# Performance work log

Hardware: AMD Instinct MI355X
Metric: run time of the kernel (lower is better)

The kernel has to match this reference:

```python
import jax, jax.numpy as jnp
import numpy as np

HIDDEN = 1024
Q_OUT = 2048
KV_OUT = 1024
HEAD_DIM = 128
N_Q = Q_OUT // HEAD_DIM      # 16
N_KV = KV_OUT // HEAD_DIM    # 8
EPS = 1e-6
ROPE_BASE = 10000.0


def _rms_norm(x, w, eps=EPS):
    # normalize over last dim (head_dim)
    ms = jnp.mean(x * x, axis=-1, keepdims=True)
    return x * jax.lax.rsqrt(ms + eps) * w


def _rope_cos_sin(t, dim=HEAD_DIM, base=ROPE_BASE):
    inv_freq = 1.0 / (base ** (jnp.arange(0, dim, 2, dtype=jnp.float32) / dim))
    pos = jnp.arange(t, dtype=jnp.float32)
    freqs = pos[:, None] * inv_freq[None, :]          # (T, D/2)
    emb = jnp.concatenate([freqs, freqs], axis=-1)    # (T, D)
    return jnp.cos(emb), jnp.sin(emb)


def _rotate_half(x):
    d = x.shape[-1] // 2
    return jnp.concatenate([-x[..., d:], x[..., :d]], axis=-1)


def setup_inputs() -> dict:
    key = jax.random.key(0)
    ks = jax.random.split(key, 7)
    def lin(k, fan_in, fan_out):
        # nn.Linear default init: U(-1/sqrt(fan_in), 1/sqrt(fan_in)); stored as (in, out) for x @ W
        bound = 1.0 / np.sqrt(fan_in)
        return jax.random.uniform(k, (fan_in, fan_out), jnp.float32, -bound, bound)
    return {
        "x": jax.random.normal(ks[0], (2, 2048, HIDDEN), jnp.float32),
        "Wq": lin(ks[1], HIDDEN, Q_OUT),
        "Wk": lin(ks[2], HIDDEN, KV_OUT),
        "Wv": lin(ks[3], HIDDEN, KV_OUT),
        "Wo": lin(ks[4], Q_OUT, HIDDEN),
        "q_norm_w": jnp.ones((HEAD_DIM,), jnp.float32),
        "k_norm_w": jnp.ones((HEAD_DIM,), jnp.float32),
    }


def reference(x, Wq, Wk, Wv, Wo, q_norm_w, k_norm_w):
    b, t, _ = x.shape
    # QKV projections, shaped to (B, H, T, D)
    q = (x @ Wq).reshape(b, t, N_Q, HEAD_DIM).transpose(0, 2, 1, 3)
    k = (x @ Wk).reshape(b, t, N_KV, HEAD_DIM).transpose(0, 2, 1, 3)
    v = (x @ Wv).reshape(b, t, N_KV, HEAD_DIM).transpose(0, 2, 1, 3)
    # per-head RMSNorm on q/k
    q = _rms_norm(q, q_norm_w)
    k = _rms_norm(k, k_norm_w)
    # RoPE (positions 0..T-1)
    cos, sin = _rope_cos_sin(t)                        # (T, D)
    cos = cos[None, None]; sin = sin[None, None]       # (1,1,T,D)
    q = q * cos + _rotate_half(q) * sin
    k = k * cos + _rotate_half(k) * sin
    # GQA: repeat_interleave kv heads to match q heads
    rep = N_Q // N_KV
    k_r = jnp.repeat(k, rep, axis=1)                   # (B, Hq, T, D)
    v_r = jnp.repeat(v, rep, axis=1)
    # causal attention
    scores = jnp.einsum('bhqd,bhkd->bhqk', q, k_r) / jnp.sqrt(jnp.asarray(HEAD_DIM, x.dtype))
    causal = jnp.triu(jnp.full((t, t), -jnp.inf, dtype=scores.dtype), k=1)[None, None]
    attn = jax.nn.softmax(scores + causal, axis=-1)
    out = jnp.einsum('bhqk,bhkd->bhqd', attn, v_r)     # (B, Hq, T, D)
    out = out.transpose(0, 2, 1, 3).reshape(b, t, Q_OUT)
    return out @ Wo
```

## Files before the change

kernel.cpp:

```cpp
#include <hip/hip_runtime.h>
#include <math.h>

typedef __attribute__((ext_vector_type(8))) short short8;
typedef __attribute__((ext_vector_type(4))) float f32x4;
typedef __attribute__((ext_vector_type(4))) unsigned int uint4v;

#define HIDDEN 1024
#define QOUT 2048
#define KVOUT 1024
#define HD 128
#define TSEQ 2048

__device__ __forceinline__ float bf2f(unsigned short h) {
    union { unsigned int u; float f; } x; x.u = ((unsigned int)h) << 16; return x.f;
}
__device__ __forceinline__ unsigned short f2bf(float f) {
    union { float f; unsigned int u; } x; x.f = f;
    unsigned int r = (x.u + 0x7fffu + ((x.u >> 16) & 1u)) >> 16;
    return (unsigned short)r;
}
__device__ __forceinline__ unsigned int pk2bf(float lo, float hi) {
    return (unsigned int)f2bf(lo) | ((unsigned int)f2bf(hi) << 16);
}

__device__ __forceinline__ void glds16(const unsigned short* g, unsigned short* l) {
    __builtin_amdgcn_global_load_lds(
        (const __attribute__((address_space(1))) unsigned int*)g,
        (__attribute__((address_space(3))) unsigned int*)l, 16, 0, 0);
}

__global__ __launch_bounds__(256) void cast_f32_bf16(const float* __restrict__ in,
                                                     unsigned short* __restrict__ out, int n4) {
    int i = blockIdx.x * 256 + threadIdx.x;
    if (i >= n4) return;
    float4 v = *(const float4*)(in + (size_t)i * 4);
    unsigned short o[4] = {f2bf(v.x), f2bf(v.y), f2bf(v.z), f2bf(v.w)};
    *(unsigned long long*)(out + (size_t)i * 4) = *(unsigned long long*)o;
}

__global__ __launch_bounds__(256) void transpose_f32_bf16(const float* __restrict__ W,
                                                          unsigned short* __restrict__ Wt,
                                                          int K, int N) {
    __shared__ __attribute__((aligned(16))) unsigned short Ls[64 * 72];
    int ntiles = N >> 6;
    int kt = blockIdx.x / ntiles, nt = blockIdx.x - kt * ntiles;
    int k0 = kt * 64, n0 = nt * 64;
    int tid = threadIdx.x;
    for (int t = 0; t < 4; t++) {
        int idx = tid + t * 256;
        int r = idx >> 4, seg = idx & 15;
        float4 v = *(const float4*)(W + (size_t)(k0 + r) * N + n0 + seg * 4);
        int c = seg * 4;
        Ls[(c + 0) * 72 + r] = f2bf(v.x);
        Ls[(c + 1) * 72 + r] = f2bf(v.y);
        Ls[(c + 2) * 72 + r] = f2bf(v.z);
        Ls[(c + 3) * 72 + r] = f2bf(v.w);
    }
    __syncthreads();
    for (int t = 0; t < 2; t++) {
        int idx = tid + t * 256;
        int rr = idx >> 3, seg = idx & 7;
        uint4v v = *(const uint4v*)(Ls + rr * 72 + seg * 8);
        *(uint4v*)(Wt + (size_t)(n0 + rr) * K + k0 + seg * 8) = v;
    }
}

template <int OUT_BF16, int BN>
__global__ __launch_bounds__(256) void gemm_bt(const unsigned short* __restrict__ A,
                                               const unsigned short* __restrict__ Bt,
                                               void* __restrict__ Cout,
                                               int M, int N, int K) {
    constexpr int MT = (BN == 128) ? 4 : 2;
    __shared__ __attribute__((aligned(16))) unsigned short As[128 * 32];
    __shared__ __attribute__((aligned(16))) unsigned short Bs[BN * 32];
    const int tid = threadIdx.x;
    const int lane = tid & 63;
    const int warp = tid >> 6;
    const int ln = lane & 15;
    const int quad = lane >> 4;
    const int wm = (BN == 128) ? (warp >> 1) : warp;
    const int wn = (BN == 128) ? (warp & 1) : 0;
    const int m0 = blockIdx.y * 128;
    const int n0 = blockIdx.x * BN;

    const int srow = lane >> 2;
    const int schunk = (lane & 3) ^ (srow & 3);
    const unsigned short* Ag = A + (size_t)(m0 + warp * 16 + srow) * K + schunk * 8;
    const unsigned short* Bg = Bt + (size_t)(n0 + warp * 16 + srow) * K + schunk * 8;
    unsigned short* AsW = As + warp * 16 * 32;
    unsigned short* BsW = Bs + warp * 16 * 32;

    f32x4 acc[MT][4];
    for (int i = 0; i < MT; i++)
        for (int j = 0; j < 4; j++) acc[i][j] = (f32x4){0.f, 0.f, 0.f, 0.f};

    const int rq = quad ^ (ln & 3);
    for (int k0 = 0; k0 < K; k0 += 32) {
        __syncthreads();
        glds16(Ag + k0, AsW);
        glds16(Ag + (size_t)64 * K + k0, AsW + 64 * 32);
        glds16(Bg + k0, BsW);
        if (BN == 128) glds16(Bg + (size_t)64 * K + k0, BsW + 64 * 32);
        __syncthreads();
        short8 af[MT], bf[4];
        for (int mt = 0; mt < MT; mt++)
            af[mt] = *(const short8*)(As + (wm * (MT * 16) + mt * 16 + ln) * 32 + rq * 8);
        for (int nt = 0; nt < 4; nt++)
            bf[nt] = *(const short8*)(Bs + (wn * 64 + nt * 16 + ln) * 32 + rq * 8);
        for (int mt = 0; mt < MT; mt++)
            for (int nt = 0; nt < 4; nt++)
                acc[mt][nt] = __builtin_amdgcn_mfma_f32_16x16x32_bf16(bf[nt], af[mt], acc[mt][nt], 0, 0, 0);
    }
    for (int mt = 0; mt < MT; mt++) {
        int row = m0 + wm * (MT * 16) + mt * 16 + ln;
        for (int nt = 0; nt < 4; nt++) {
            int colb = n0 + wn * 64 + nt * 16 + quad * 4;
            if (OUT_BF16) {
                unsigned long long pk =
                    (unsigned long long)pk2bf(acc[mt][nt][0], acc[mt][nt][1]) |
                    ((unsigned long long)pk2bf(acc[mt][nt][2], acc[mt][nt][3]) << 32);
                *(unsigned long long*)((unsigned short*)Cout + (size_t)row * N + colb) = pk;
            } else {
                *(f32x4*)((float*)Cout + (size_t)row * N + colb) = acc[mt][nt];
            }
        }
    }
}

__global__ __launch_bounds__(256) void norm_rope(const unsigned short* __restrict__ QKV,
                                                 const float* __restrict__ qw,
                                                 const float* __restrict__ kw,
                                                 unsigned short* __restrict__ Q,
                                                 unsigned short* __restrict__ Kb) {
    int warp = threadIdx.x >> 6;
    int lane = threadIdx.x & 63;
    int gid = blockIdx.x * 4 + warp;
    int tok = gid / 24;
    int slot = gid - tok * 24;
    int b = tok >> 11, t = tok & 2047;
    const float* w;
    unsigned short* dst;
    int col0;
    if (slot < 16) {
        col0 = slot * HD;
        dst = Q + ((size_t)(b * 16 + slot) * TSEQ + t) * HD;
        w = qw;
    } else {
        int hk = slot - 16;
        col0 = QOUT + hk * HD;
        dst = Kb + ((size_t)(b * 8 + hk) * TSEQ + t) * HD;
        w = kw;
    }
    const unsigned short* row = QKV + (size_t)tok * 4096 + col0;
    float e0 = bf2f(row[lane]), e1 = bf2f(row[lane + 64]);
    float ss = e0 * e0 + e1 * e1;
    for (int off = 1; off < 64; off <<= 1) ss += __shfl_xor(ss, off);
    float rr = rsqrtf(ss * (1.0f / 128.0f) + 1e-6f);
    float n0 = e0 * rr * w[lane];
    float n1 = e1 * rr * w[lane + 64];
    float invf = __builtin_exp2f(-(float)lane * 0.20762050593045951f);
    float ang = (float)t * invf;
    float sf, cf;
    __sincosf(ang, &sf, &cf);
    float o0 = n0 * cf - n1 * sf;
    float o1 = n1 * cf + n0 * sf;
    dst[lane] = f2bf(o0);
    dst[lane + 64] = f2bf(o1);
}

__global__ __launch_bounds__(256) void v_transpose(const unsigned short* __restrict__ QKV,
                                                   unsigned short* __restrict__ Vt) {
    __shared__ __attribute__((aligned(16))) unsigned short Ls[128 * 72];
    int bid = blockIdx.x;
    int tt = bid & 31, hk = (bid >> 5) & 7, b = bid >> 8;
    int t0 = tt * 64;
    int tid = threadIdx.x;
    const unsigned short* base = QKV + (size_t)(b * 2048 + t0) * 4096 + 3072 + hk * 128;
    for (int i = 0; i < 4; i++) {
        int idx = tid + i * 256;
        int r = idx >> 4, seg = idx & 15;
        uint4v v = *(const uint4v*)(base + (size_t)r * 4096 + seg * 8);
        unsigned short* pv = (unsigned short*)&v;
        int d = seg * 8;
        for (int jj = 0; jj < 8; jj++) Ls[(d + jj) * 72 + r] = pv[jj];
    }
    __syncthreads();
    unsigned short* out = Vt + (size_t)(b * 8 + hk) * 128 * 2048;
    for (int i = 0; i < 4; i++) {
        int idx = tid + i * 256;
        int d = idx >> 3, seg = idx & 7;
        uint4v v = *(const uint4v*)(Ls + d * 72 + seg * 8);
        *(uint4v*)(out + (size_t)d * 2048 + t0 + seg * 8) = v;
    }
}

__global__ __launch_bounds__(256, 2) void attn(const unsigned short* __restrict__ Q,
                                               const unsigned short* __restrict__ Kg,
                                               const unsigned short* __restrict__ Vt,
                                               unsigned short* __restrict__ Og) {
    __shared__ __attribute__((aligned(16))) unsigned short Ks[64 * 128];
    __shared__ __attribute__((aligned(16))) unsigned short Vs[128 * 64];
    __shared__ __attribute__((aligned(16))) unsigned short Ps[4][16 * 72];
    const int p = blockIdx.x;
    const int bh = blockIdx.y;
    const int b = bh >> 4, h = bh & 15, hk = h >> 1;
    const int tid = threadIdx.x;
    const int warp = tid >> 6, lane = tid & 63, ln = lane & 15, quad = lane >> 4;
    const int strip[2] = { p * 64 + warp * 16, (31 - p) * 64 + warp * 16 };
    const int jdiag[2] = { p, 31 - p };

    const unsigned short* Kbase = Kg + (size_t)(b * 8 + hk) * TSEQ * HD;
    const unsigned short* Vbase = Vt + (size_t)(b * 8 + hk) * HD * TSEQ;
    const unsigned short* Qh = Q + (size_t)(b * 16 + h) * TSEQ * HD;

    short8 qf[2][4];
#pragma unroll
    for (int st = 0; st < 2; st++)
#pragma unroll
        for (int kt = 0; kt < 4; kt++)
            qf[st][kt] = *(const short8*)(Qh + (size_t)(strip[st] + ln) * HD + kt * 32 + quad * 8);

    f32x4 o[2][8];
#pragma unroll
    for (int st = 0; st < 2; st++)
#pragma unroll
        for (int ot = 0; ot < 8; ot++) o[st][ot] = (f32x4){0.f, 0.f, 0.f, 0.f};
    float m_[2] = {-1e30f, -1e30f}, l_[2] = {0.f, 0.f};

    const int kr = lane >> 4;
    const int kc = lane & 15;
    const int vr = lane >> 3;
    const int vc = lane & 7;

    const float kscale = 0.12750580997495268f;
    const int nT = 32 - p;
    for (int j = 0; j < nT; j++) {
        const int j0 = j * 64;
        __syncthreads();
#pragma unroll
        for (int c = 0; c < 4; c++) {
            int row = warp * 16 + c * 4 + kr;
            glds16(Kbase + (size_t)(j0 + row) * HD + ((kc ^ (row & 15)) * 8),
                   Ks + (warp * 16 + c * 4) * 128);
        }
#pragma unroll
        for (int c = 0; c < 4; c++) {
            int d = warp * 32 + c * 8 + vr;
            glds16(Vbase + (size_t)d * TSEQ + j0 + ((vc ^ (d & 7)) * 8),
                   Vs + (warp * 32 + c * 8) * 64);
        }
        __syncthreads();
        const bool act0 = (j <= jdiag[0]);
        f32x4 s[2][4];
#pragma unroll
        for (int kb = 0; kb < 4; kb++) {
            s[0][kb] = (f32x4){0.f, 0.f, 0.f, 0.f};
            s[1][kb] = (f32x4){0.f, 0.f, 0.f, 0.f};
        }
#pragma unroll
        for (int kt = 0; kt < 4; kt++) {
            short8 kf[4];
#pragma unroll
            for (int kb = 0; kb < 4; kb++)
                kf[kb] = *(const short8*)(Ks + (kb * 16 + ln) * 128 + (((kt * 4 + quad) ^ ln) * 8));
#pragma unroll
            for (int kb = 0; kb < 4; kb++)
                s[1][kb] = __builtin_amdgcn_mfma_f32_16x16x32_bf16(kf[kb], qf[1][kt], s[1][kb], 0, 0, 0);
            if (act0)
#pragma unroll
                for (int kb = 0; kb < 4; kb++)
                    s[0][kb] = __builtin_amdgcn_mfma_f32_16x16x32_bf16(kf[kb], qf[0][kt], s[0][kb], 0, 0, 0);
        }
        short8 pf[2][2];
        float al[2] = {1.f, 1.f};
#pragma unroll
        for (int st = 0; st < 2; st++) {
            if (st == 0 && !act0) continue;
            float mx = -1e30f;
            if (j == jdiag[st]) {
                const int qloc = warp * 16 + ln;
#pragma unroll
                for (int kb = 0; kb < 4; kb++)
#pragma unroll
                    for (int r = 0; r < 4; r++) {
                        int kvloc = kb * 16 + quad * 4 + r;
                        float v = s[st][kb][r] * kscale;
                        v = (kvloc > qloc) ? -1e30f : v;
                        s[st][kb][r] = v;
                        mx = fmaxf(mx, v);
                    }
            } else {
#pragma unroll
                for (int kb = 0; kb < 4; kb++)
#pragma unroll
                    for (int r = 0; r < 4; r++) {
                        float v = s[st][kb][r] * kscale;
                        s[st][kb][r] = v;
                        mx = fmaxf(mx, v);
                    }
            }
            mx = fmaxf(mx, __shfl_xor(mx, 16));
            mx = fmaxf(mx, __shfl_xor(mx, 32));
            float mn = fmaxf(m_[st], mx);
            al[st] = __builtin_exp2f(m_[st] - mn);
            float sum = 0.f;
#pragma unroll
            for (int kb = 0; kb < 4; kb++)
#pragma unroll
                for (int r = 0; r < 4; r++) {
                    float pv = __builtin_exp2f(s[st][kb][r] - mn);
                    s[st][kb][r] = pv;
                    sum += pv;
                }
            sum += __shfl_xor(sum, 16);
            sum += __shfl_xor(sum, 32);
            m_[st] = mn;
            l_[st] = l_[st] * al[st] + sum;
#pragma unroll
            for (int kb = 0; kb < 4; kb++) {
                unsigned long long pk =
                    (unsigned long long)pk2bf(s[st][kb][0], s[st][kb][1]) |
                    ((unsigned long long)pk2bf(s[st][kb][2], s[st][kb][3]) << 32);
                *(unsigned long long*)(&Ps[warp][ln * 72 + kb * 16 + quad * 4]) = pk;
            }
            pf[st][0] = *(const short8*)(&Ps[warp][ln * 72 + quad * 8]);
            pf[st][1] = *(const short8*)(&Ps[warp][ln * 72 + 32 + quad * 8]);
        }
        if (act0 && __any(al[0] != 1.0f))
#pragma unroll
            for (int ot = 0; ot < 8; ot++)
#pragma unroll
                for (int r = 0; r < 4; r++) o[0][ot][r] *= al[0];
        if (__any(al[1] != 1.0f))
#pragma unroll
            for (int ot = 0; ot < 8; ot++)
#pragma unroll
                for (int r = 0; r < 4; r++) o[1][ot][r] *= al[1];
#pragma unroll
        for (int ot = 0; ot < 8; ot++) {
            short8 vf0 = *(const short8*)(Vs + (ot * 16 + ln) * 64 + ((quad ^ (ln & 7)) * 8));
            short8 vf1 = *(const short8*)(Vs + (ot * 16 + ln) * 64 + (((4 + quad) ^ (ln & 7)) * 8));
            o[1][ot] = __builtin_amdgcn_mfma_f32_16x16x32_bf16(vf0, pf[1][0], o[1][ot], 0, 0, 0);
            o[1][ot] = __builtin_amdgcn_mfma_f32_16x16x32_bf16(vf1, pf[1][1], o[1][ot], 0, 0, 0);
            if (act0) {
                o[0][ot] = __builtin_amdgcn_mfma_f32_16x16x32_bf16(vf0, pf[0][0], o[0][ot], 0, 0, 0);
                o[0][ot] = __builtin_amdgcn_mfma_f32_16x16x32_bf16(vf1, pf[0][1], o[0][ot], 0, 0, 0);
            }
        }
    }
#pragma unroll
    for (int st = 0; st < 2; st++) {
        float inv = 1.0f / l_[st];
        size_t rowoff = ((size_t)(b * TSEQ + strip[st] + ln)) * QOUT + h * 128 + quad * 4;
#pragma unroll
        for (int ot = 0; ot < 8; ot++) {
            unsigned long long pk =
                (unsigned long long)pk2bf(o[st][ot][0] * inv, o[st][ot][1] * inv) |
                ((unsigned long long)pk2bf(o[st][ot][2] * inv, o[st][ot][3] * inv) << 32);
            *(unsigned long long*)(Og + rowoff + ot * 16) = pk;
        }
    }
}

extern "C" void kernel_launch(void* const* d_in, const int* in_sizes, int n_in,
                              void* d_out, int out_size, void* d_ws, size_t ws_size,
                              hipStream_t stream) {
    (void)in_sizes; (void)n_in; (void)out_size;
    const float* x  = (const float*)d_in[0];
    const float* Wq = (const float*)d_in[1];
    const float* Wk = (const float*)d_in[2];
    const float* Wv = (const float*)d_in[3];
    const float* Wo = (const float*)d_in[4];
    const float* qw = (const float*)d_in[5];
    const float* kw = (const float*)d_in[6];

    char* ws = (char*)d_ws;
    const size_t MB = 1024 * 1024;
    unsigned short* Wt   = (unsigned short*)(ws);
    unsigned short* Wot  = (unsigned short*)(ws + 8 * MB);
    unsigned short* QKVb = (unsigned short*)(ws + 12 * MB);
    unsigned short* xb   = (unsigned short*)(ws + 44 * MB);
    unsigned short* Qb   = (unsigned short*)(ws + 52 * MB);
    unsigned short* Kb   = (unsigned short*)(ws + 68 * MB);
    unsigned short* Vtb  = (unsigned short*)(ws + 76 * MB);
    unsigned short* Ob   = (unsigned short*)(ws + 84 * MB);
    if (ws_size < 100 * MB) return;

    cast_f32_bf16<<<dim3(4096), 256, 0, stream>>>(x, xb, 1048576);
    transpose_f32_bf16<<<dim3(512), 256, 0, stream>>>(Wq, Wt, 1024, 2048);
    transpose_f32_bf16<<<dim3(256), 256, 0, stream>>>(Wk, Wt + (size_t)2048 * 1024, 1024, 1024);
    transpose_f32_bf16<<<dim3(256), 256, 0, stream>>>(Wv, Wt + (size_t)3072 * 1024, 1024, 1024);
    transpose_f32_bf16<<<dim3(512), 256, 0, stream>>>(Wo, Wot, 2048, 1024);
    gemm_bt<1, 128><<<dim3(32, 32), 256, 0, stream>>>(xb, Wt, QKVb, 4096, 4096, 1024);
    norm_rope<<<dim3(24576), 256, 0, stream>>>(QKVb, qw, kw, Qb, Kb);
    v_transpose<<<dim3(512), 256, 0, stream>>>(QKVb, Vtb);
    attn<<<dim3(16, 32), 256, 0, stream>>>(Qb, Kb, Vtb, Ob);
    gemm_bt<0, 64><<<dim3(16, 32), 256, 0, stream>>>(Ob, Wot, (float*)d_out, 4096, 1024, 2048);
}
```

Measured before the change: 300.9 us.

## Double-buffer LDS in GEMM and attention and merge small prep kernels

```diff
diff --git a/kernel.cpp b/kernel.cpp
--- a/kernel.cpp
+++ b/kernel.cpp
@@ -29,23 +29,33 @@
         (__attribute__((address_space(3))) unsigned int*)l, 16, 0, 0);
 }
 
-__global__ __launch_bounds__(256) void cast_f32_bf16(const float* __restrict__ in,
-                                                     unsigned short* __restrict__ out, int n4) {
-    int i = blockIdx.x * 256 + threadIdx.x;
-    if (i >= n4) return;
-    float4 v = *(const float4*)(in + (size_t)i * 4);
-    unsigned short o[4] = {f2bf(v.x), f2bf(v.y), f2bf(v.z), f2bf(v.w)};
-    *(unsigned long long*)(out + (size_t)i * 4) = *(unsigned long long*)o;
-}
-
-__global__ __launch_bounds__(256) void transpose_f32_bf16(const float* __restrict__ W,
-                                                          unsigned short* __restrict__ Wt,
-                                                          int K, int N) {
+__global__ __launch_bounds__(256) void prep(const float* __restrict__ x,
+                                            const float* __restrict__ Wq,
+                                            const float* __restrict__ Wk,
+                                            const float* __restrict__ Wv,
+                                            const float* __restrict__ Wo,
+                                            unsigned short* __restrict__ xb,
+                                            unsigned short* __restrict__ Wt,
+                                            unsigned short* __restrict__ Wot) {
+    int bid = blockIdx.x;
+    int tid = threadIdx.x;
+    if (bid < 4096) {
+        int i = bid * 256 + tid;
+        float4 v = *(const float4*)(x + (size_t)i * 4);
+        unsigned short o[4] = {f2bf(v.x), f2bf(v.y), f2bf(v.z), f2bf(v.w)};
+        *(unsigned long long*)(xb + (size_t)i * 4) = *(unsigned long long*)o;
+        return;
+    }
+    bid -= 4096;
+    const float* W; unsigned short* D; int K, N;
+    if (bid < 512)       { W = Wq; D = Wt;                          K = 1024; N = 2048; }
+    else if (bid < 768)  { bid -= 512;  W = Wk; D = Wt + (size_t)2048 * 1024; K = 1024; N = 1024; }
+    else if (bid < 1024) { bid -= 768;  W = Wv; D = Wt + (size_t)3072 * 1024; K = 1024; N = 1024; }
+    else                 { bid -= 1024; W = Wo; D = Wot;                      K = 2048; N = 1024; }
     __shared__ __attribute__((aligned(16))) unsigned short Ls[64 * 72];
     int ntiles = N >> 6;
-    int kt = blockIdx.x / ntiles, nt = blockIdx.x - kt * ntiles;
+    int kt = bid / ntiles, nt = bid - kt * ntiles;
     int k0 = kt * 64, n0 = nt * 64;
-    int tid = threadIdx.x;
     for (int t = 0; t < 4; t++) {
         int idx = tid + t * 256;
         int r = idx >> 4, seg = idx & 15;
@@ -61,7 +71,7 @@
         int idx = tid + t * 256;
         int rr = idx >> 3, seg = idx & 7;
         uint4v v = *(const uint4v*)(Ls + rr * 72 + seg * 8);
-        *(uint4v*)(Wt + (size_t)(n0 + rr) * K + k0 + seg * 8) = v;
+        *(uint4v*)(D + (size_t)(n0 + rr) * K + k0 + seg * 8) = v;
     }
 }
 
@@ -71,8 +81,8 @@
                                                void* __restrict__ Cout,
                                                int M, int N, int K) {
     constexpr int MT = (BN == 128) ? 4 : 2;
-    __shared__ __attribute__((aligned(16))) unsigned short As[128 * 32];
-    __shared__ __attribute__((aligned(16))) unsigned short Bs[BN * 32];
+    __shared__ __attribute__((aligned(16))) unsigned short As[2][128 * 32];
+    __shared__ __attribute__((aligned(16))) unsigned short Bs[2][BN * 32];
     const int tid = threadIdx.x;
     const int lane = tid & 63;
     const int warp = tid >> 6;
@@ -87,32 +97,45 @@
     const int schunk = (lane & 3) ^ (srow & 3);
     const unsigned short* Ag = A + (size_t)(m0 + warp * 16 + srow) * K + schunk * 8;
     const unsigned short* Bg = Bt + (size_t)(n0 + warp * 16 + srow) * K + schunk * 8;
-    unsigned short* AsW = As + warp * 16 * 32;
-    unsigned short* BsW = Bs + warp * 16 * 32;
 
     f32x4 acc[MT][4];
+#pragma unroll
     for (int i = 0; i < MT; i++)
+#pragma unroll
         for (int j = 0; j < 4; j++) acc[i][j] = (f32x4){0.f, 0.f, 0.f, 0.f};
 
+    auto stage = [&](int k0, int bi) {
+        glds16(Ag + k0, As[bi] + warp * 16 * 32);
+        glds16(Ag + (size_t)64 * K + k0, As[bi] + warp * 16 * 32 + 64 * 32);
+        glds16(Bg + k0, Bs[bi] + warp * 16 * 32);
+        if (BN == 128) glds16(Bg + (size_t)64 * K + k0, Bs[bi] + warp * 16 * 32 + 64 * 32);
+    };
+
     const int rq = quad ^ (ln & 3);
-    for (int k0 = 0; k0 < K; k0 += 32) {
+    const int KI = K >> 5;
+    stage(0, 0);
+    for (int it = 0; it < KI; it++) {
         __syncthreads();
-        glds16(Ag + k0, AsW);
-        glds16(Ag + (size_t)64 * K + k0, AsW + 64 * 32);
-        glds16(Bg + k0, BsW);
-        if (BN == 128) glds16(Bg + (size_t)64 * K + k0, BsW + 64 * 32);
-        __syncthreads();
+        if (it + 1 < KI) stage((it + 1) << 5, (it + 1) & 1);
+        const unsigned short* Ab = As[it & 1];
+        const unsigned short* Bb = Bs[it & 1];
         short8 af[MT], bf[4];
+#pragma unroll
         for (int mt = 0; mt < MT; mt++)
-            af[mt] = *(const short8*)(As + (wm * (MT * 16) + mt * 16 + ln) * 32 + rq * 8);
+            af[mt] = *(const short8*)(Ab + (wm * (MT * 16) + mt * 16 + ln) * 32 + rq * 8);
+#pragma unroll
         for (int nt = 0; nt < 4; nt++)
-            bf[nt] = *(const short8*)(Bs + (wn * 64 + nt * 16 + ln) * 32 + rq * 8);
+            bf[nt] = *(const short8*)(Bb + (wn * 64 + nt * 16 + ln) * 32 + rq * 8);
+#pragma unroll
         for (int mt = 0; mt < MT; mt++)
+#pragma unroll
             for (int nt = 0; nt < 4; nt++)
                 acc[mt][nt] = __builtin_amdgcn_mfma_f32_16x16x32_bf16(bf[nt], af[mt], acc[mt][nt], 0, 0, 0);
     }
+#pragma unroll
     for (int mt = 0; mt < MT; mt++) {
         int row = m0 + wm * (MT * 16) + mt * 16 + ln;
+#pragma unroll
         for (int nt = 0; nt < 4; nt++) {
             int colb = n0 + wn * 64 + nt * 16 + quad * 4;
             if (OUT_BF16) {
@@ -127,51 +150,49 @@
     }
 }
 
-__global__ __launch_bounds__(256) void norm_rope(const unsigned short* __restrict__ QKV,
-                                                 const float* __restrict__ qw,
-                                                 const float* __restrict__ kw,
-                                                 unsigned short* __restrict__ Q,
-                                                 unsigned short* __restrict__ Kb) {
-    int warp = threadIdx.x >> 6;
-    int lane = threadIdx.x & 63;
-    int gid = blockIdx.x * 4 + warp;
-    int tok = gid / 24;
-    int slot = gid - tok * 24;
-    int b = tok >> 11, t = tok & 2047;
-    const float* w;
-    unsigned short* dst;
-    int col0;
-    if (slot < 16) {
-        col0 = slot * HD;
-        dst = Q + ((size_t)(b * 16 + slot) * TSEQ + t) * HD;
-        w = qw;
-    } else {
-        int hk = slot - 16;
-        col0 = QOUT + hk * HD;
-        dst = Kb + ((size_t)(b * 8 + hk) * TSEQ + t) * HD;
-        w = kw;
-    }
-    const unsigned short* row = QKV + (size_t)tok * 4096 + col0;
-    float e0 = bf2f(row[lane]), e1 = bf2f(row[lane + 64]);
-    float ss = e0 * e0 + e1 * e1;
-    for (int off = 1; off < 64; off <<= 1) ss += __shfl_xor(ss, off);
-    float rr = rsqrtf(ss * (1.0f / 128.0f) + 1e-6f);
-    float n0 = e0 * rr * w[lane];
-    float n1 = e1 * rr * w[lane + 64];
-    float invf = __builtin_exp2f(-(float)lane * 0.20762050593045951f);
-    float ang = (float)t * invf;
-    float sf, cf;
-    __sincosf(ang, &sf, &cf);
-    float o0 = n0 * cf - n1 * sf;
-    float o1 = n1 * cf + n0 * sf;
-    dst[lane] = f2bf(o0);
-    dst[lane + 64] = f2bf(o1);
-}
-
-__global__ __launch_bounds__(256) void v_transpose(const unsigned short* __restrict__ QKV,
-                                                   unsigned short* __restrict__ Vt) {
+__global__ __launch_bounds__(256) void nrvt(const unsigned short* __restrict__ QKV,
+                                            const float* __restrict__ qw,
+                                            const float* __restrict__ kw,
+                                            unsigned short* __restrict__ Q,
+                                            unsigned short* __restrict__ Kb,
+                                            unsigned short* __restrict__ Vt) {
+    if (blockIdx.x < 24576) {
+        int warp = threadIdx.x >> 6;
+        int lane = threadIdx.x & 63;
+        int gid = blockIdx.x * 4 + warp;
+        int tok = gid / 24;
+        int slot = gid - tok * 24;
+        int b = tok >> 11, t = tok & 2047;
+        const float* w;
+        unsigned short* dst;
+        int col0;
+        if (slot < 16) {
+            col0 = slot * HD;
+            dst = Q + ((size_t)(b * 16 + slot) * TSEQ + t) * HD;
+            w = qw;
+        } else {
+            int hk = slot - 16;
+            col0 = QOUT + hk * HD;
+            dst = Kb + ((size_t)(b * 8 + hk) * TSEQ + t) * HD;
+            w = kw;
+        }
+        const unsigned short* row = QKV + (size_t)tok * 4096 + col0;
+        float e0 = bf2f(row[lane]), e1 = bf2f(row[lane + 64]);
+        float ss = e0 * e0 + e1 * e1;
+        for (int off = 1; off < 64; off <<= 1) ss += __shfl_xor(ss, off);
+        float rr = rsqrtf(ss * (1.0f / 128.0f) + 1e-6f);
+        float n0 = e0 * rr * w[lane];
+        float n1 = e1 * rr * w[lane + 64];
+        float invf = __builtin_exp2f(-(float)lane * 0.20762050593045951f);
+        float ang = (float)t * invf;
+        float sf, cf;
+        __sincosf(ang, &sf, &cf);
+        dst[lane] = f2bf(n0 * cf - n1 * sf);
+        dst[lane + 64] = f2bf(n1 * cf + n0 * sf);
+        return;
+    }
     __shared__ __attribute__((aligned(16))) unsigned short Ls[128 * 72];
-    int bid = blockIdx.x;
+    int bid = blockIdx.x - 24576;
     int tt = bid & 31, hk = (bid >> 5) & 7, b = bid >> 8;
     int t0 = tt * 64;
     int tid = threadIdx.x;
@@ -198,8 +219,8 @@
                                                const unsigned short* __restrict__ Kg,
                                                const unsigned short* __restrict__ Vt,
                                                unsigned short* __restrict__ Og) {
-    __shared__ __attribute__((aligned(16))) unsigned short Ks[64 * 128];
-    __shared__ __attribute__((aligned(16))) unsigned short Vs[128 * 64];
+    __shared__ __attribute__((aligned(16))) unsigned short Ks[2][64 * 128];
+    __shared__ __attribute__((aligned(16))) unsigned short Vs[2][128 * 64];
     __shared__ __attribute__((aligned(16))) unsigned short Ps[4][16 * 72];
     const int p = blockIdx.x;
     const int bh = blockIdx.y;
@@ -232,24 +253,32 @@
     const int vr = lane >> 3;
     const int vc = lane & 7;
 
+    auto stage_kv = [&](int jt, int bi) {
+        const int j0s = jt * 64;
+        unsigned short* KsB = Ks[bi];
+        unsigned short* VsB = Vs[bi];
+#pragma unroll
+        for (int c = 0; c < 4; c++) {
+            int row = warp * 16 + c * 4 + kr;
+            glds16(Kbase + (size_t)(j0s + row) * HD + ((kc ^ (row & 15)) * 8),
+                   KsB + (warp * 16 + c * 4) * 128);
+        }
+#pragma unroll
+        for (int c = 0; c < 4; c++) {
+            int d = warp * 32 + c * 8 + vr;
+            glds16(Vbase + (size_t)d * TSEQ + j0s + ((vc ^ (d & 7)) * 8),
+                   VsB + (warp * 32 + c * 8) * 64);
+        }
+    };
+
     const float kscale = 0.12750580997495268f;
     const int nT = 32 - p;
+    stage_kv(0, 0);
     for (int j = 0; j < nT; j++) {
-        const int j0 = j * 64;
         __syncthreads();
-#pragma unroll
-        for (int c = 0; c < 4; c++) {
-            int row = warp * 16 + c * 4 + kr;
-            glds16(Kbase + (size_t)(j0 + row) * HD + ((kc ^ (row & 15)) * 8),
-                   Ks + (warp * 16 + c * 4) * 128);
-        }
-#pragma unroll
-        for (int c = 0; c < 4; c++) {
-            int d = warp * 32 + c * 8 + vr;
-            glds16(Vbase + (size_t)d * TSEQ + j0 + ((vc ^ (d & 7)) * 8),
-                   Vs + (warp * 32 + c * 8) * 64);
-        }
-        __syncthreads();
+        if (j + 1 < nT) stage_kv(j + 1, (j + 1) & 1);
+        const unsigned short* KsC = Ks[j & 1];
+        const unsigned short* VsC = Vs[j & 1];
         const bool act0 = (j <= jdiag[0]);
         f32x4 s[2][4];
 #pragma unroll
@@ -262,7 +291,7 @@
             short8 kf[4];
 #pragma unroll
             for (int kb = 0; kb < 4; kb++)
-                kf[kb] = *(const short8*)(Ks + (kb * 16 + ln) * 128 + (((kt * 4 + quad) ^ ln) * 8));
+                kf[kb] = *(const short8*)(KsC + (kb * 16 + ln) * 128 + (((kt * 4 + quad) ^ ln) * 8));
 #pragma unroll
             for (int kb = 0; kb < 4; kb++)
                 s[1][kb] = __builtin_amdgcn_mfma_f32_16x16x32_bf16(kf[kb], qf[1][kt], s[1][kb], 0, 0, 0);
@@ -338,8 +367,8 @@
                 for (int r = 0; r < 4; r++) o[1][ot][r] *= al[1];
 #pragma unroll
         for (int ot = 0; ot < 8; ot++) {
-            short8 vf0 = *(const short8*)(Vs + (ot * 16 + ln) * 64 + ((quad ^ (ln & 7)) * 8));
-            short8 vf1 = *(const short8*)(Vs + (ot * 16 + ln) * 64 + (((4 + quad) ^ (ln & 7)) * 8));
+            short8 vf0 = *(const short8*)(VsC + (ot * 16 + ln) * 64 + ((quad ^ (ln & 7)) * 8));
+            short8 vf1 = *(const short8*)(VsC + (ot * 16 + ln) * 64 + (((4 + quad) ^ (ln & 7)) * 8));
             o[1][ot] = __builtin_amdgcn_mfma_f32_16x16x32_bf16(vf0, pf[1][0], o[1][ot], 0, 0, 0);
             o[1][ot] = __builtin_amdgcn_mfma_f32_16x16x32_bf16(vf1, pf[1][1], o[1][ot], 0, 0, 0);
             if (act0) {
@@ -386,14 +415,9 @@
     unsigned short* Ob   = (unsigned short*)(ws + 84 * MB);
     if (ws_size < 100 * MB) return;
 
-    cast_f32_bf16<<<dim3(4096), 256, 0, stream>>>(x, xb, 1048576);
-    transpose_f32_bf16<<<dim3(512), 256, 0, stream>>>(Wq, Wt, 1024, 2048);
-    transpose_f32_bf16<<<dim3(256), 256, 0, stream>>>(Wk, Wt + (size_t)2048 * 1024, 1024, 1024);
-    transpose_f32_bf16<<<dim3(256), 256, 0, stream>>>(Wv, Wt + (size_t)3072 * 1024, 1024, 1024);
-    transpose_f32_bf16<<<dim3(512), 256, 0, stream>>>(Wo, Wot, 2048, 1024);
+    prep<<<dim3(5632), 256, 0, stream>>>(x, Wq, Wk, Wv, Wo, xb, Wt, Wot);
     gemm_bt<1, 128><<<dim3(32, 32), 256, 0, stream>>>(xb, Wt, QKVb, 4096, 4096, 1024);
-    norm_rope<<<dim3(24576), 256, 0, stream>>>(QKVb, qw, kw, Qb, Kb);
-    v_transpose<<<dim3(512), 256, 0, stream>>>(QKVb, Vtb);
+    nrvt<<<dim3(25088), 256, 0, stream>>>(QKVb, qw, kw, Qb, Kb, Vtb);
     attn<<<dim3(16, 32), 256, 0, stream>>>(Qb, Kb, Vtb, Ob);
     gemm_bt<0, 64><<<dim3(16, 32), 256, 0, stream>>>(Ob, Wot, (float*)d_out, 4096, 1024, 2048);
 }
```

After: 286.2 us. 4.9% less time.
